# Performance work log

Hardware: AMD Instinct MI355X
Metric: run time of the kernel (lower is better)

## Reference

```python
import jax, jax.numpy as jnp
import numpy as np

B, S, D, H = 2, 2048, 1024, 16
DH = D // H
LN_EPS = 1e-12


def setup_inputs() -> dict:
    key = jax.random.key(0)
    ks = jax.random.split(key, 11)
    s = 0.02
    return {
        "hidden_states": jax.random.normal(ks[0], (B, S, D), dtype=jnp.float32),
        "Wq": jax.random.normal(ks[1], (D, D), dtype=jnp.float32) * s,
        "bq": jnp.zeros((D,), jnp.float32),
        "Wk": jax.random.normal(ks[2], (D, D), dtype=jnp.float32) * s,
        "bk": jnp.zeros((D,), jnp.float32),
        "Wv": jax.random.normal(ks[3], (D, D), dtype=jnp.float32) * s,
        "bv": jnp.zeros((D,), jnp.float32),
        "Wd": jax.random.normal(ks[4], (D, D), dtype=jnp.float32) * s,  # torch Linear weight [out,in]
        "bd": jnp.zeros((D,), jnp.float32),
        "ln_g": jnp.ones((D,), jnp.float32),
        "ln_b": jnp.zeros((D,), jnp.float32),
    }


def reference(hidden_states, Wq, bq, Wk, bk, Wv, bv, Wd, bd, ln_g, ln_b):
    x = hidden_states  # [B,S,D]
    # torch Linear: y = x @ W.T + b
    def heads(y):
        return y.reshape(B, S, H, DH).transpose(0, 2, 1, 3)  # [B,H,S,DH]

    q = heads(x @ Wq.T + bq)
    k = heads(x @ Wk.T + bk)
    v = heads(x @ Wv.T + bv)

    scores = jnp.einsum('bhsd,bhtd->bhst', q, k) / jnp.sqrt(jnp.float32(DH))
    probs = jax.nn.softmax(scores, axis=-1)  # [B,H,S,S]
    ctx = jnp.einsum('bhst,bhtd->bshd', probs, v)  # [B,S,H,DH]

    # fused output projection: einsum('bfnd,ndh->bfh') with w = Wd.T reshaped
    w = Wd.T.reshape(H, DH, D)
    proj = jnp.einsum('bfnd,ndh->bfh', ctx, w) + bd  # [B,S,D]

    mu = jnp.mean(proj, axis=-1, keepdims=True)
    var = jnp.var(proj, axis=-1, keepdims=True)
    out = (proj - mu) / jnp.sqrt(var + LN_EPS) * ln_g + ln_b
    return out
```

## Files before the change

kernel.cpp:

```cpp
#include <hip/hip_runtime.h>

#define HD 16
#define DHEAD 64
#define DMODEL 1024
#define BB 2
#define SS 2048
#define MTOT (BB*SS)
#define LOG2E 1.44269504f

typedef float f32x4 __attribute__((ext_vector_type(4)));
typedef float f32x16 __attribute__((ext_vector_type(16)));
typedef __bf16 bf16x8 __attribute__((ext_vector_type(8)));
typedef unsigned short u16x8 __attribute__((ext_vector_type(8)));
typedef unsigned int u32x2 __attribute__((ext_vector_type(2)));
typedef unsigned int u32x4 __attribute__((ext_vector_type(4)));

__device__ __forceinline__ unsigned short f2bf(float f) {
    unsigned int u = __builtin_bit_cast(unsigned int, f);
    unsigned int r = (u + 0x7fffu + ((u >> 16) & 1u)) >> 16;
    return (unsigned short)r;
}

__device__ __forceinline__ float bf2f(unsigned short u) {
    return __builtin_bit_cast(float, ((unsigned int)u) << 16);
}

__device__ __forceinline__ bf16x8 ld8(const unsigned short* p) {
    u16x8 v = *reinterpret_cast<const u16x8*>(p);
    return __builtin_bit_cast(bf16x8, v);
}

__device__ __forceinline__ void gload_lds16b(const char* g, char* l) {
    __builtin_amdgcn_global_load_lds(
        (const __attribute__((address_space(1))) void*)g,
        (__attribute__((address_space(3))) void*)l, 16, 0, 0);
}

__device__ __forceinline__ unsigned cvt_pk_bf16(float lo, float hi) {
    unsigned r;
    asm("v_cvt_pk_bf16_f32 %0, %1, %2" : "=v"(r) : "v"(lo), "v"(hi));
    return r;
}

__global__ __launch_bounds__(256) void cvt_all(
    const float* __restrict__ x,
    const float* __restrict__ w0, const float* __restrict__ w1,
    const float* __restrict__ w2, const float* __restrict__ w3,
    unsigned short* __restrict__ xb,
    unsigned short* __restrict__ o0, unsigned short* __restrict__ o1,
    unsigned short* __restrict__ o2, unsigned short* __restrict__ o3) {
    int y = blockIdx.y;
    const float* in;
    unsigned short* out;
    int idx;
    if (y < 4) {
        in  = (y == 0) ? w0 : (y == 1) ? w1 : (y == 2) ? w2 : w3;
        out = (y == 0) ? o0 : (y == 1) ? o1 : (y == 2) ? o2 : o3;
        idx = blockIdx.x * 256 + threadIdx.x;
    } else {
        in  = x;
        out = xb;
        idx = ((y - 4) * 1024 + blockIdx.x) * 256 + threadIdx.x;
    }
    float4 v = reinterpret_cast<const float4*>(in)[idx];
    ushort4 o;
    o.x = f2bf(v.x); o.y = f2bf(v.y); o.z = f2bf(v.z); o.w = f2bf(v.w);
    reinterpret_cast<ushort4*>(out)[idx] = o;
}

__global__ __launch_bounds__(256, 2) void gemm_qkv(
    const unsigned short* __restrict__ xb,
    const unsigned short* __restrict__ Wqb, const unsigned short* __restrict__ Wkb,
    const unsigned short* __restrict__ Wvb,
    const float* __restrict__ bq, const float* __restrict__ bk, const float* __restrict__ bv,
    unsigned short* __restrict__ Qo, unsigned short* __restrict__ Ko, unsigned short* __restrict__ VTo) {
    __shared__ unsigned short Als[2][8192];
    __shared__ unsigned short Bls[2][8192];
    int L = blockIdx.x;
    int wg = (L & 7) * 96 + (L >> 3);
    int z = wg >> 8, rem = wg & 255;
    int n0 = (rem & 7) * 128, m0 = (rem >> 3) * 128;
    const unsigned short* Bm = (z == 0) ? Wqb : (z == 1) ? Wkb : Wvb;
    const float* bias = (z == 0) ? bq : (z == 1) ? bk : bv;

    int t = threadIdx.x, wv = t >> 6, lane = t & 63;
    int q5 = lane & 31, hi = lane >> 5;
    int wm = wv >> 1, wn = wv & 1;
    const char* Ac = (const char*)xb;
    const char* Bc = (const char*)Bm;

    auto stage = [&](int bf, int k0) {
#pragma unroll
        for (int i = 0; i < 4; ++i) {
            int c = t + 256 * i;
            int kr = c >> 3, kc = ((c & 7) << 4) ^ ((kr & 7) << 4);
            gload_lds16b(Ac + ((size_t)(m0 + kr) * DMODEL + k0) * 2 + kc, (char*)&Als[bf][0] + c * 16);
        }
#pragma unroll
        for (int i = 0; i < 4; ++i) {
            int c = t + 256 * i;
            int kr = c >> 3, kc = ((c & 7) << 4) ^ ((kr & 7) << 4);
            gload_lds16b(Bc + ((size_t)(n0 + kr) * DMODEL + k0) * 2 + kc, (char*)&Bls[bf][0] + c * 16);
        }
    };

    f32x16 acc[2][2];
#pragma unroll
    for (int fm = 0; fm < 2; ++fm)
#pragma unroll
        for (int fn = 0; fn < 2; ++fn) acc[fm][fn] = (f32x16)0.f;

    stage(0, 0);
    int buf = 0;
    for (int k0 = 0; k0 < DMODEL; k0 += 64) {
        __builtin_amdgcn_s_barrier();
        if (k0 + 64 < DMODEL) {
            stage(buf ^ 1, k0 + 64);
            asm volatile("s_waitcnt vmcnt(8)" ::: "memory");
        } else {
            asm volatile("s_waitcnt vmcnt(0)" ::: "memory");
        }
        __builtin_amdgcn_sched_barrier(0);
        __builtin_amdgcn_s_barrier();
        __builtin_amdgcn_sched_barrier(0);

        const char* als = (const char*)&Als[buf][0];
        const char* bls = (const char*)&Bls[buf][0];
        __builtin_amdgcn_s_setprio(1);
#pragma unroll
        for (int ks = 0; ks < 4; ++ks) {
            int kb = ks * 32 + hi * 16;
            bf16x8 af[2], bfr[2];
#pragma unroll
            for (int fm = 0; fm < 2; ++fm) {
                int row = wm * 64 + fm * 32 + q5;
                af[fm] = *reinterpret_cast<const bf16x8*>(als + row * 128 + (kb ^ ((row & 7) << 4)));
            }
#pragma unroll
            for (int fn = 0; fn < 2; ++fn) {
                int row = wn * 64 + fn * 32 + q5;
                bfr[fn] = *reinterpret_cast<const bf16x8*>(bls + row * 128 + (kb ^ ((row & 7) << 4)));
            }
#pragma unroll
            for (int fm = 0; fm < 2; ++fm)
#pragma unroll
                for (int fn = 0; fn < 2; ++fn)
                    acc[fm][fn] = __builtin_amdgcn_mfma_f32_32x32x16_bf16(af[fm], bfr[fn], acc[fm][fn], 0, 0, 0);
        }
        __builtin_amdgcn_s_setprio(0);
        buf ^= 1;
    }

    float scale = (z == 0) ? (0.125f * LOG2E) : 1.0f;
    int b = m0 >> 11;
#pragma unroll
    for (int fm = 0; fm < 2; ++fm) {
#pragma unroll
        for (int fn = 0; fn < 2; ++fn) {
            int col = n0 + wn * 64 + fn * 32 + q5;
            int h = col >> 6, dh = col & 63;
            float bi = bias[col];
            if (z == 2) {
#pragma unroll
                for (int rq = 0; rq < 4; ++rq) {
                    int s0 = ((m0 + wm * 64 + fm * 32 + 8 * rq + 4 * hi) & 2047);
                    ushort4 pk;
                    pk.x = f2bf(acc[fm][fn][4 * rq + 0] + bi);
                    pk.y = f2bf(acc[fm][fn][4 * rq + 1] + bi);
                    pk.z = f2bf(acc[fm][fn][4 * rq + 2] + bi);
                    pk.w = f2bf(acc[fm][fn][4 * rq + 3] + bi);
                    *reinterpret_cast<ushort4*>(&VTo[((size_t)((b * HD + h) * DHEAD + dh)) * SS + s0]) = pk;
                }
            } else {
                unsigned short* o = (z == 0) ? Qo : Ko;
#pragma unroll
                for (int r = 0; r < 16; ++r) {
                    int s = (m0 + wm * 64 + fm * 32 + (r & 3) + 8 * (r >> 2) + 4 * hi) & 2047;
                    o[((size_t)((b * HD + h) * SS + s)) * DHEAD + dh] = f2bf((acc[fm][fn][r] + bi) * scale);
                }
            }
        }
    }
}

__global__ __launch_bounds__(256, 2) void attn_kernel(
    const unsigned short* __restrict__ Qb, const unsigned short* __restrict__ Kb,
    const unsigned short* __restrict__ VTb, unsigned short* __restrict__ ctxo) {
    __shared__ char smem[4][16384];
    int L = blockIdx.x + (int)gridDim.x * blockIdx.y;
    int wg = (L & 7) * 64 + (L >> 3);
    int q0 = (wg & 15) * 128;
    int bh = wg >> 4;
    int t = threadIdx.x, wv = t >> 6, lane = t & 63;
    int q5 = lane & 31, hi = lane >> 5;
    const unsigned short* Qh  = Qb  + (size_t)bh * SS * DHEAD;
    const char* Khc  = (const char*)(Kb  + (size_t)bh * SS * DHEAD);
    const char* VThc = (const char*)(VTb + (size_t)bh * DHEAD * SS);
    int qr = q0 + wv * 32;

    bf16x8 qf[4];
#pragma unroll
    for (int m = 0; m < 4; ++m)
        qf[m] = ld8(&Qh[(size_t)(qr + q5) * DHEAD + m * 16 + hi * 8]);

    const __bf16 one_bf = (__bf16)1.0f;
    bf16x8 ones8 = {one_bf, one_bf, one_bf, one_bf, one_bf, one_bf, one_bf, one_bf};

    f32x16 oo[2];
    oo[0] = (f32x16)0.f; oo[1] = (f32x16)0.f;
    f32x16 ls = (f32x16)0.f;
    float mrun = 0.f;

    auto stage = [&](int ph) {
        char* kb = smem[ph & 3];
        char* vb = kb + 8192;
        int t0 = ph * 64;
#pragma unroll
        for (int i = 0; i < 2; ++i) {
            int c = t + 256 * i;
            int kr = c >> 3, kc = ((c & 7) << 4) ^ ((kr & 7) << 4);
            gload_lds16b(Khc + (size_t)(t0 + kr) * 128 + kc, kb + c * 16);
        }
#pragma unroll
        for (int i = 0; i < 2; ++i) {
            int c = t + 256 * i;
            int vr = c >> 3, vc = ((c & 7) << 4) ^ ((vr & 7) << 4);
            gload_lds16b(VThc + ((size_t)vr * SS + t0) * 2 + vc, vb + c * 16);
        }
    };

    stage(0); stage(1); stage(2);

    for (int ph = 0; ph < 32; ++ph) {
        if (ph < 30)       asm volatile("s_waitcnt vmcnt(8)" ::: "memory");
        else if (ph == 30) asm volatile("s_waitcnt vmcnt(4)" ::: "memory");
        else               asm volatile("s_waitcnt vmcnt(0)" ::: "memory");
        __builtin_amdgcn_sched_barrier(0);
        __builtin_amdgcn_s_barrier();
        __builtin_amdgcn_sched_barrier(0);

        if (ph + 3 < 32) stage(ph + 3);

        const char* kls = smem[ph & 3];
        const char* vls = kls + 8192;

        f32x16 sc[2];
        __builtin_amdgcn_s_setprio(1);
#pragma unroll
        for (int tb = 0; tb < 2; ++tb) {
            int row = tb * 32 + q5;
            int rsw = (row & 7) << 4;
            f32x16 s = (f32x16)(-mrun);
#pragma unroll
            for (int m = 0; m < 4; ++m) {
                bf16x8 kf = *reinterpret_cast<const bf16x8*>(kls + row * 128 + ((m * 32 + hi * 16) ^ rsw));
                s = __builtin_amdgcn_mfma_f32_32x32x16_bf16(kf, qf[m], s, 0, 0, 0);
            }
            sc[tb] = s;
        }
        __builtin_amdgcn_s_setprio(0);

        float tm[11];
#pragma unroll
        for (int i = 0; i < 10; ++i) {
            float a0 = (3 * i < 16)     ? sc[0][3 * i]      : sc[1][3 * i - 16];
            float a1 = (3 * i + 1 < 16) ? sc[0][3 * i + 1]  : sc[1][3 * i + 1 - 16];
            float a2 = (3 * i + 2 < 16) ? sc[0][3 * i + 2]  : sc[1][3 * i + 2 - 16];
            tm[i] = fmaxf(fmaxf(a0, a1), a2);
        }
        tm[10] = fmaxf(sc[1][14], sc[1][15]);
        float u0 = fmaxf(fmaxf(tm[0], tm[1]), tm[2]);
        float u1 = fmaxf(fmaxf(tm[3], tm[4]), tm[5]);
        float u2 = fmaxf(fmaxf(tm[6], tm[7]), tm[8]);
        float u3 = fmaxf(tm[9], tm[10]);
        float lm = fmaxf(fmaxf(fmaxf(u0, u1), u2), u3);

        if (__any(lm > 8.f)) {
            u32x2 sw = __builtin_amdgcn_permlane32_swap(__builtin_bit_cast(unsigned, lm),
                                                        __builtin_bit_cast(unsigned, lm), false, false);
            float rowmax = fmaxf(__builtin_bit_cast(float, sw[0]), __builtin_bit_cast(float, sw[1]));
            float d = fmaxf(rowmax, 0.f);
            float al = exp2f(-d);
            mrun += d;
#pragma unroll
            for (int r = 0; r < 16; ++r) {
                float alr = __shfl(al, (r & 3) + 8 * (r >> 2) + 4 * hi);
                oo[0][r] *= alr; oo[1][r] *= alr; ls[r] *= alr;
            }
#pragma unroll
            for (int tb = 0; tb < 2; ++tb)
#pragma unroll
                for (int r = 0; r < 16; ++r)
                    sc[tb][r] -= d;
        }

#pragma unroll
        for (int tb = 0; tb < 2; ++tb)
#pragma unroll
            for (int r = 0; r < 16; ++r)
                sc[tb][r] = exp2f(sc[tb][r]);

        u32x4 paw[4];
#pragma unroll
        for (int tb = 0; tb < 2; ++tb)
#pragma unroll
            for (int u2i = 0; u2i < 2; ++u2i)
#pragma unroll
                for (int e = 0; e < 2; ++e) {
                    unsigned wd = cvt_pk_bf16(sc[tb][8 * u2i + 2 * e], sc[tb][8 * u2i + 2 * e + 1]);
                    unsigned ws = cvt_pk_bf16(sc[tb][8 * u2i + 4 + 2 * e], sc[tb][8 * u2i + 4 + 2 * e + 1]);
                    u32x2 rr = __builtin_amdgcn_permlane32_swap(wd, ws, false, false);
                    paw[tb * 2 + u2i][e] = rr[0];
                    paw[tb * 2 + u2i][2 + e] = rr[1];
                }

        __builtin_amdgcn_s_setprio(1);
#pragma unroll
        for (int dblk = 0; dblk < 2; ++dblk) {
            int row = dblk * 32 + q5;
            int rsw = (row & 7) << 4;
#pragma unroll
            for (int ks = 0; ks < 4; ++ks) {
                bf16x8 vf = *reinterpret_cast<const bf16x8*>(
                    vls + row * 128 + ((ks * 32 + hi * 16) ^ rsw));
                oo[dblk] = __builtin_amdgcn_mfma_f32_32x32x16_bf16(
                    __builtin_bit_cast(bf16x8, paw[ks]), vf, oo[dblk], 0, 0, 0);
            }
        }
#pragma unroll
        for (int ks = 0; ks < 4; ++ks)
            ls = __builtin_amdgcn_mfma_f32_32x32x16_bf16(
                __builtin_bit_cast(bf16x8, paw[ks]), ones8, ls, 0, 0, 0);
        __builtin_amdgcn_s_setprio(0);
    }

    int b = bh >> 4, h = bh & 15;
#pragma unroll
    for (int r = 0; r < 16; ++r) {
        float invr = 1.f / ls[r];
        int qrel = (r & 3) + 8 * (r >> 2) + 4 * hi;
        int s = qr + qrel;
        size_t base = ((size_t)(b * SS + s)) * DMODEL + h * DHEAD;
        ctxo[base + q5]      = f2bf(oo[0][r] * invr);
        ctxo[base + 32 + q5] = f2bf(oo[1][r] * invr);
    }
}

__global__ __launch_bounds__(256, 2) void gemm_proj(
    const unsigned short* __restrict__ ctxb, const unsigned short* __restrict__ Wdb,
    const float* __restrict__ bd, unsigned short* __restrict__ projb) {
    __shared__ unsigned short Als[2][8192];
    __shared__ unsigned short Bls[2][4096];
    int L = blockIdx.x;
    int wg = (L & 7) * 64 + (L >> 3);
    int n0 = (wg & 15) * 64, m0 = (wg >> 4) * 128;

    int t = threadIdx.x, wv = t >> 6, lane = t & 63;
    int q5 = lane & 31, hi = lane >> 5;
    int wm = wv >> 1, wn = wv & 1;
    const char* Ac = (const char*)ctxb;
    const char* Bc = (const char*)Wdb;

    auto stage = [&](int bf, int k0) {
#pragma unroll
        for (int i = 0; i < 4; ++i) {
            int c = t + 256 * i;
            int kr = c >> 3, kc = ((c & 7) << 4) ^ ((kr & 7) << 4);
            gload_lds16b(Ac + ((size_t)(m0 + kr) * DMODEL + k0) * 2 + kc, (char*)&Als[bf][0] + c * 16);
        }
#pragma unroll
        for (int i = 0; i < 2; ++i) {
            int c = t + 256 * i;
            int kr = c >> 3, kc = ((c & 7) << 4) ^ ((kr & 7) << 4);
            gload_lds16b(Bc + ((size_t)(n0 + kr) * DMODEL + k0) * 2 + kc, (char*)&Bls[bf][0] + c * 16);
        }
    };

    f32x16 acc[2];
    acc[0] = (f32x16)0.f; acc[1] = (f32x16)0.f;

    stage(0, 0);
    int buf = 0;
    for (int k0 = 0; k0 < DMODEL; k0 += 64) {
        __builtin_amdgcn_s_barrier();
        if (k0 + 64 < DMODEL) {
            stage(buf ^ 1, k0 + 64);
            asm volatile("s_waitcnt vmcnt(6)" ::: "memory");
        } else {
            asm volatile("s_waitcnt vmcnt(0)" ::: "memory");
        }
        __builtin_amdgcn_sched_barrier(0);
        __builtin_amdgcn_s_barrier();
        __builtin_amdgcn_sched_barrier(0);

        const char* als = (const char*)&Als[buf][0];
        const char* bls = (const char*)&Bls[buf][0];
        __builtin_amdgcn_s_setprio(1);
#pragma unroll
        for (int ks = 0; ks < 4; ++ks) {
            int kb = ks * 32 + hi * 16;
            bf16x8 af[2], bfr;
#pragma unroll
            for (int fm = 0; fm < 2; ++fm) {
                int row = wm * 64 + fm * 32 + q5;
                af[fm] = *reinterpret_cast<const bf16x8*>(als + row * 128 + (kb ^ ((row & 7) << 4)));
            }
            {
                int row = wn * 32 + q5;
                bfr = *reinterpret_cast<const bf16x8*>(bls + row * 128 + (kb ^ ((row & 7) << 4)));
            }
#pragma unroll
            for (int fm = 0; fm < 2; ++fm)
                acc[fm] = __builtin_amdgcn_mfma_f32_32x32x16_bf16(af[fm], bfr, acc[fm], 0, 0, 0);
        }
        __builtin_amdgcn_s_setprio(0);
        buf ^= 1;
    }

    int col = n0 + wn * 32 + q5;
    float bi = bd[col];
#pragma unroll
    for (int fm = 0; fm < 2; ++fm)
#pragma unroll
        for (int r = 0; r < 16; ++r) {
            int row = m0 + wm * 64 + fm * 32 + (r & 3) + 8 * (r >> 2) + 4 * hi;
            projb[(size_t)row * DMODEL + col] = f2bf(acc[fm][r] + bi);
        }
}

__global__ __launch_bounds__(256) void ln_kernel(const unsigned short* __restrict__ projb,
                                                 const float* __restrict__ g,
                                                 const float* __restrict__ bv,
                                                 float* __restrict__ out) {
    int row = blockIdx.x, t = threadIdx.x;
    ushort4 u = reinterpret_cast<const ushort4*>(projb + (size_t)row * DMODEL)[t];
    float4 v;
    v.x = bf2f(u.x); v.y = bf2f(u.y); v.z = bf2f(u.z); v.w = bf2f(u.w);
    float s  = v.x + v.y + v.z + v.w;
    float s2 = v.x * v.x + v.y * v.y + v.z * v.z + v.w * v.w;
#pragma unroll
    for (int m = 1; m < 64; m <<= 1) { s += __shfl_xor(s, m); s2 += __shfl_xor(s2, m); }
    __shared__ float red[8];
    int wv = t >> 6, lane = t & 63;
    if (lane == 0) { red[wv] = s; red[wv + 4] = s2; }
    __syncthreads();
    s  = red[0] + red[1] + red[2] + red[3];
    s2 = red[4] + red[5] + red[6] + red[7];
    float mu  = s * (1.f / 1024.f);
    float var = s2 * (1.f / 1024.f) - mu * mu;
    float inv = rsqrtf(var + 1e-12f);
    float4 gv = reinterpret_cast<const float4*>(g)[t];
    float4 bb = reinterpret_cast<const float4*>(bv)[t];
    float4 ov;
    ov.x = (v.x - mu) * inv * gv.x + bb.x;
    ov.y = (v.y - mu) * inv * gv.y + bb.y;
    ov.z = (v.z - mu) * inv * gv.z + bb.z;
    ov.w = (v.w - mu) * inv * gv.w + bb.w;
    reinterpret_cast<float4*>(out + (size_t)row * DMODEL)[t] = ov;
}

extern "C" void kernel_launch(void* const* d_in, const int* in_sizes, int n_in,
                              void* d_out, int out_size, void* d_ws, size_t ws_size,
                              hipStream_t stream) {
    const float* x   = (const float*)d_in[0];
    const float* Wq  = (const float*)d_in[1];
    const float* bq  = (const float*)d_in[2];
    const float* Wk  = (const float*)d_in[3];
    const float* bk  = (const float*)d_in[4];
    const float* Wv  = (const float*)d_in[5];
    const float* bv  = (const float*)d_in[6];
    const float* Wd  = (const float*)d_in[7];
    const float* bd  = (const float*)d_in[8];
    const float* lng = (const float*)d_in[9];
    const float* lnb = (const float*)d_in[10];

    char* ws = (char*)d_ws;
    unsigned short* xb    = (unsigned short*)(ws);
    unsigned short* Wqb   = (unsigned short*)(ws + (8u  << 20));
    unsigned short* Wkb   = (unsigned short*)(ws + (10u << 20));
    unsigned short* Wvb   = (unsigned short*)(ws + (12u << 20));
    unsigned short* Wdb   = (unsigned short*)(ws + (14u << 20));
    unsigned short* Qb    = (unsigned short*)(ws + (16u << 20));
    unsigned short* Kb    = (unsigned short*)(ws + (24u << 20));
    unsigned short* VTb   = (unsigned short*)(ws + (32u << 20));
    unsigned short* ctxb  = (unsigned short*)(ws + (40u << 20));
    unsigned short* projb = (unsigned short*)(ws + (16u << 20));

    cvt_all<<<dim3(1024, 8), 256, 0, stream>>>(x, Wq, Wk, Wv, Wd, xb, Wqb, Wkb, Wvb, Wdb);
    gemm_qkv<<<768, 256, 0, stream>>>(xb, Wqb, Wkb, Wvb, bq, bk, bv, Qb, Kb, VTb);
    attn_kernel<<<dim3(16, 32), 256, 0, stream>>>(Qb, Kb, VTb, ctxb);
    gemm_proj<<<512, 256, 0, stream>>>(ctxb, Wdb, bd, projb);
    ln_kernel<<<4096, 256, 0, stream>>>(projb, lng, lnb, (float*)d_out);
}
```

Measured before the change: 135.1 us.

## Software-pipeline QK^T of next KV tile with softmax of current tile

Restructures the attention inner loop so the QK^T MFMAs for tile ph+1 are issued right after the barrier, before the softmax, exp and PV work of tile ph. Two score register sets are used in ping-pong fashion, and the loop is unrolled by two. Wait counts are tightened so tile ph+1 is resident in LDS at iteration ph. When a running-max rescale happens, the scores already computed for the next tile are also shifted, which keeps the result correct. The goal is to overlap matrix-core work with the VALU-heavy softmax. The cost is 32 more live accumulator registers per lane, which could lower occupancy or cause spills.

```diff
diff --git a/kernel.cpp b/kernel.cpp
--- a/kernel.cpp
+++ b/kernel.cpp
@@ -229,22 +229,8 @@
         }
     };
 
-    stage(0); stage(1); stage(2);
-
-    for (int ph = 0; ph < 32; ++ph) {
-        if (ph < 30)       asm volatile("s_waitcnt vmcnt(8)" ::: "memory");
-        else if (ph == 30) asm volatile("s_waitcnt vmcnt(4)" ::: "memory");
-        else               asm volatile("s_waitcnt vmcnt(0)" ::: "memory");
-        __builtin_amdgcn_sched_barrier(0);
-        __builtin_amdgcn_s_barrier();
-        __builtin_amdgcn_sched_barrier(0);
-
-        if (ph + 3 < 32) stage(ph + 3);
-
-        const char* kls = smem[ph & 3];
-        const char* vls = kls + 8192;
-
-        f32x16 sc[2];
+    auto qk_into = [&](int php, f32x16 (&scn)[2]) {
+        const char* kls = smem[php & 3];
         __builtin_amdgcn_s_setprio(1);
 #pragma unroll
         for (int tb = 0; tb < 2; ++tb) {
@@ -256,19 +242,39 @@
                 bf16x8 kf = *reinterpret_cast<const bf16x8*>(kls + row * 128 + ((m * 32 + hi * 16) ^ rsw));
                 s = __builtin_amdgcn_mfma_f32_32x32x16_bf16(kf, qf[m], s, 0, 0, 0);
             }
-            sc[tb] = s;
+            scn[tb] = s;
         }
         __builtin_amdgcn_s_setprio(0);
+    };
+
+    f32x16 scA[2], scB[2];
+
+    stage(0); stage(1); stage(2);
+    asm volatile("s_waitcnt vmcnt(8)" ::: "memory");
+    __builtin_amdgcn_sched_barrier(0);
+    __builtin_amdgcn_s_barrier();
+    __builtin_amdgcn_sched_barrier(0);
+    qk_into(0, scA);
+
+    auto body = [&](int ph, f32x16 (&scc)[2], f32x16 (&scn)[2]) {
+        if (ph < 30) asm volatile("s_waitcnt vmcnt(4)" ::: "memory");
+        else         asm volatile("s_waitcnt vmcnt(0)" ::: "memory");
+        __builtin_amdgcn_sched_barrier(0);
+        __builtin_amdgcn_s_barrier();
+        __builtin_amdgcn_sched_barrier(0);
+
+        if (ph + 3 < 32) stage(ph + 3);
+        if (ph + 1 < 32) qk_into(ph + 1, scn);
 
         float tm[11];
 #pragma unroll
         for (int i = 0; i < 10; ++i) {
-            float a0 = (3 * i < 16)     ? sc[0][3 * i]      : sc[1][3 * i - 16];
-            float a1 = (3 * i + 1 < 16) ? sc[0][3 * i + 1]  : sc[1][3 * i + 1 - 16];
-            float a2 = (3 * i + 2 < 16) ? sc[0][3 * i + 2]  : sc[1][3 * i + 2 - 16];
+            float a0 = (3 * i < 16)     ? scc[0][3 * i]      : scc[1][3 * i - 16];
+            float a1 = (3 * i + 1 < 16) ? scc[0][3 * i + 1]  : scc[1][3 * i + 1 - 16];
+            float a2 = (3 * i + 2 < 16) ? scc[0][3 * i + 2]  : scc[1][3 * i + 2 - 16];
             tm[i] = fmaxf(fmaxf(a0, a1), a2);
         }
-        tm[10] = fmaxf(sc[1][14], sc[1][15]);
+        tm[10] = fmaxf(scc[1][14], scc[1][15]);
         float u0 = fmaxf(fmaxf(tm[0], tm[1]), tm[2]);
         float u1 = fmaxf(fmaxf(tm[3], tm[4]), tm[5]);
         float u2 = fmaxf(fmaxf(tm[6], tm[7]), tm[8]);
@@ -290,15 +296,17 @@
 #pragma unroll
             for (int tb = 0; tb < 2; ++tb)
 #pragma unroll
-                for (int r = 0; r < 16; ++r)
-                    sc[tb][r] -= d;
+                for (int r = 0; r < 16; ++r) {
+                    scc[tb][r] -= d;
+                    scn[tb][r] -= d;
+                }
         }
 
 #pragma unroll
         for (int tb = 0; tb < 2; ++tb)
 #pragma unroll
             for (int r = 0; r < 16; ++r)
-                sc[tb][r] = exp2f(sc[tb][r]);
+                scc[tb][r] = exp2f(scc[tb][r]);
 
         u32x4 paw[4];
 #pragma unroll
@@ -307,13 +315,14 @@
             for (int u2i = 0; u2i < 2; ++u2i)
 #pragma unroll
                 for (int e = 0; e < 2; ++e) {
-                    unsigned wd = cvt_pk_bf16(sc[tb][8 * u2i + 2 * e], sc[tb][8 * u2i + 2 * e + 1]);
-                    unsigned ws = cvt_pk_bf16(sc[tb][8 * u2i + 4 + 2 * e], sc[tb][8 * u2i + 4 + 2 * e + 1]);
+                    unsigned wd = cvt_pk_bf16(scc[tb][8 * u2i + 2 * e], scc[tb][8 * u2i + 2 * e + 1]);
+                    unsigned ws = cvt_pk_bf16(scc[tb][8 * u2i + 4 + 2 * e], scc[tb][8 * u2i + 4 + 2 * e + 1]);
                     u32x2 rr = __builtin_amdgcn_permlane32_swap(wd, ws, false, false);
                     paw[tb * 2 + u2i][e] = rr[0];
                     paw[tb * 2 + u2i][2 + e] = rr[1];
                 }
 
+        const char* vls = smem[ph & 3] + 8192;
         __builtin_amdgcn_s_setprio(1);
 #pragma unroll
         for (int dblk = 0; dblk < 2; ++dblk) {
@@ -332,6 +341,11 @@
             ls = __builtin_amdgcn_mfma_f32_32x32x16_bf16(
                 __builtin_bit_cast(bf16x8, paw[ks]), ones8, ls, 0, 0, 0);
         __builtin_amdgcn_s_setprio(0);
+    };
+
+    for (int pp = 0; pp < 16; ++pp) {
+        body(2 * pp,     scA, scB);
+        body(2 * pp + 1, scB, scA);
     }
 
     int b = bh >> 4, h = bh & 15;
```

Result: no change. 135.0 us, median of 2 (-0.0%).
